# Kernel tuning notes

Hardware: AMD Instinct MI355X
Metric: run time of the kernel (lower is better)

The kernel has to match this reference:

```python
import jax, jax.numpy as jnp
import numpy as np

H = 256          # hidden_size
D = 2 * H        # GRU state size
ODE_H = 128      # ode_hidden_dim
IN_U = 32        # input_size - 1 (dt channel stripped)
OUT = 16         # output_size
L, B = 128, 1024


def setup_inputs() -> dict:
    key = jax.random.key(0)
    ks = jax.random.split(key, 16)
    s = lambda k, shape, fan: jax.random.normal(k, shape, jnp.float32) * (1.0 / np.sqrt(fan))
    ext = jax.random.uniform(ks[0], (L, B, IN_U + 1), jnp.float32)  # last channel = dt > 0
    obs = jax.random.normal(ks[1], (L, B, OUT), jnp.float32)
    return {
        "external_input_seq": ext,
        "observations_seq": obs,
        # PreProcess (Linear + tanh)
        "Wu": s(ks[2], (IN_U, H), IN_U), "bu": jnp.zeros((H,), jnp.float32),
        "Wx": s(ks[3], (OUT, H), OUT), "bx": jnp.zeros((H,), jnp.float32),
        # GRUCell(2H -> 2H), torch layout: [3*D, D]
        "W_ih": s(ks[4], (3 * D, D), D), "W_hh": s(ks[5], (3 * D, D), D),
        "b_ih": jnp.zeros((3 * D,), jnp.float32), "b_hh": jnp.zeros((3 * D,), jnp.float32),
        # ODE gradient net: Linear(H,ODE_H) -> tanh -> Linear(ODE_H,H)
        "W1": s(ks[6], (H, ODE_H), H), "b1": jnp.zeros((ODE_H,), jnp.float32),
        "W2": s(ks[7], (ODE_H, H), ODE_H), "b2": jnp.zeros((H,), jnp.float32),
        # Ly: Linear(2H, OUT)
        "WLy": s(ks[8], (D, OUT), D), "bLy": jnp.zeros((OUT,), jnp.float32),
    }


def _forward(external_input_seq, observations_seq, Wu, bu, Wx, bx,
             W_ih, W_hh, b_ih, b_hh, W1, b1, W2, b2, WLy, bLy):
    ext = external_input_seq[..., :-1]            # (L,B,IN_U)
    dt = external_input_seq[..., -1]              # (L,B)
    u_emb = jnp.tanh(ext @ Wu + bu)               # (L,B,H)
    x_emb = jnp.tanh(observations_seq @ Wx + bx)  # (L,B,H)

    def gru(x, h):
        gi = x @ W_ih.T + b_ih                    # (B,3D)
        gh = h @ W_hh.T + b_hh
        r = jax.nn.sigmoid(gi[:, :D] + gh[:, :D])
        z = jax.nn.sigmoid(gi[:, D:2 * D] + gh[:, D:2 * D])
        n = jnp.tanh(gi[:, 2 * D:] + r * gh[:, 2 * D:])
        return (1.0 - z) * n + z * h

    def step(hn, inp):
        u_t, x_t, dt_t = inp
        hn_new = gru(jnp.concatenate([u_t, x_t], axis=-1), hn)
        h, c = hn_new[:, :H], hn_new[:, H:]
        # Euler ODE step over [0, dt]: h <- h + dt * f(h)
        f = jnp.tanh(h @ W1 + b1) @ W2 + b2
        h = h + dt_t[:, None] * f
        hn_out = jnp.concatenate([h, c], axis=-1)
        return hn_out, hn  # h_seq collects carry BEFORE update (h_seq[:-1] semantics)

    hn0 = jnp.zeros((external_input_seq.shape[1], D), external_input_seq.dtype)
    _, h_seq = jax.lax.scan(step, hn0, (u_emb, x_emb, dt))  # (L,B,D)
    x_seq = h_seq @ WLy + bLy                               # (L,B,OUT) == state_mu
    return x_seq


def reference(external_input_seq, observations_seq, Wu, bu, Wx, bx,
              W_ih, W_hh, b_ih, b_hh, W1, b1, W2, b2, WLy, bLy):
    return _forward(external_input_seq, observations_seq, Wu, bu, Wx, bx,
                    W_ih, W_hh, b_ih, b_hh, W1, b1, W2, b2, WLy, bLy)
```

## Files before the change

### kernel.cpp

```cpp
#include <hip/hip_runtime.h>

#define LSEQ 128
#define BATCH 1024
#define DDIM 512
#define G3 1536
#define HS ((size_t)BATCH * DDIM)
#define INV2048 4.8828125e-4f
#define WST 520

typedef _Float16 h8 __attribute__((ext_vector_type(8)));
typedef float floatx4 __attribute__((ext_vector_type(4)));

#define MFMA16(acc, A, B) acc = __builtin_amdgcn_mfma_f32_16x16x32_f16(A, B, acc, 0, 0, 0)

__device__ __forceinline__ void fsplitS(float x, _Float16* hi, _Float16* lo) {
    _Float16 h = (_Float16)x;
    *hi = h;
    *lo = (_Float16)((x - (float)h) * 2048.0f);
}

#define BAR_LEAF(i) ((i) * 32)
#define BAR_MID(i)  ((64 + (i)) * 32)
#define BAR_ROOT    (72 * 32)
#define BAR_GEN     (73 * 32)
#define BAR_WORDS   4096

__device__ __forceinline__ void grid_bar(unsigned* bar, int blk, unsigned epoch) {
    __syncthreads();
    if (threadIdx.x == 0) {
        __builtin_amdgcn_fence(__ATOMIC_RELEASE, "agent");
        const int leaf = blk >> 2;
        unsigned v = __hip_atomic_fetch_add(bar + BAR_LEAF(leaf), 1u, __ATOMIC_ACQ_REL, __HIP_MEMORY_SCOPE_AGENT);
        if (v + 1u == epoch * 4u) {
            const int mid = leaf >> 3;
            unsigned m = __hip_atomic_fetch_add(bar + BAR_MID(mid), 1u, __ATOMIC_ACQ_REL, __HIP_MEMORY_SCOPE_AGENT);
            if (m + 1u == epoch * 8u) {
                unsigned r = __hip_atomic_fetch_add(bar + BAR_ROOT, 1u, __ATOMIC_ACQ_REL, __HIP_MEMORY_SCOPE_AGENT);
                if (r + 1u == epoch * 8u) {
                    __hip_atomic_store(bar + BAR_GEN, epoch, __ATOMIC_RELEASE, __HIP_MEMORY_SCOPE_AGENT);
                }
            }
        }
        while (__hip_atomic_load(bar + BAR_GEN, __ATOMIC_RELAXED, __HIP_MEMORY_SCOPE_AGENT) < epoch)
            __builtin_amdgcn_s_sleep(2);
        __builtin_amdgcn_fence(__ATOMIC_ACQUIRE, "agent");
    }
    __syncthreads();
}

__global__ void prep_kernel(const float* __restrict__ Wih,
                            const float* __restrict__ W1, const float* __restrict__ W2,
                            const float* __restrict__ WLy,
                            _Float16* __restrict__ Wih_lo,
                            _Float16* __restrict__ W1T_hi, _Float16* __restrict__ W1T_lo,
                            _Float16* __restrict__ W2T_hi, _Float16* __restrict__ W2T_lo,
                            _Float16* __restrict__ WLyT_hi, _Float16* __restrict__ WLyT_lo,
                            float* __restrict__ hn_f32, _Float16* __restrict__ hn_hi,
                            _Float16* __restrict__ hn_lo, unsigned* __restrict__ bar)
{
    int tid = blockIdx.x * 256 + threadIdx.x;
    for (int i = tid; i < G3 * DDIM; i += 65536) { _Float16 h; fsplitS(Wih[i], &h, &Wih_lo[i]); }
    for (int i = tid; i < 128 * 256; i += 65536) { int n = i >> 8, k = i & 255; fsplitS(W1[k * 128 + n], &W1T_hi[i], &W1T_lo[i]); }
    for (int i = tid; i < 256 * 128; i += 65536) { int n = i >> 7, k = i & 127; fsplitS(W2[k * 256 + n], &W2T_hi[i], &W2T_lo[i]); }
    for (int i = tid; i < 16 * 512;  i += 65536) { int n = i >> 9, k = i & 511; fsplitS(WLy[k * 16 + n], &WLyT_hi[i], &WLyT_lo[i]); }
    for (int i = tid; i < BATCH * DDIM; i += 65536) { hn_f32[i] = 0.f; hn_hi[i] = (_Float16)0.f; hn_lo[i] = (_Float16)0.f; }
    for (int i = tid; i < BAR_WORDS; i += 65536) bar[i] = 0u;
}

__device__ __forceinline__ void embed_rows(const float* __restrict__ ext, const float* __restrict__ obs,
                                           const float* __restrict__ Wu, const float* __restrict__ bu,
                                           const float* __restrict__ Wx, const float* __restrict__ bx,
                                           int t, int r0, int tid, float* stg,
                                           _Float16* __restrict__ oh, _Float16* __restrict__ ol)
{
    for (int i = tid; i < 256; i += 512) stg[i] = ext[((size_t)t * BATCH + r0 + (i >> 5)) * 33 + (i & 31)];
    for (int i = tid; i < 128; i += 512) stg[256 + i] = obs[((size_t)t * BATCH + r0 + (i >> 4)) * 16 + (i & 15)];
    __syncthreads();
    int c = tid;
    if (c < 256) {
        float wv[32];
        #pragma unroll
        for (int k = 0; k < 32; ++k) wv[k] = Wu[k * 256 + c];
        float b = bu[c];
        for (int r = 0; r < 8; ++r) {
            float acc = b;
            #pragma unroll
            for (int k = 0; k < 32; ++k) acc += stg[r * 32 + k] * wv[k];
            size_t p = (size_t)(r0 + r) * DDIM + c;
            fsplitS(tanhf(acc), &oh[p], &ol[p]);
        }
    } else {
        int cc = c - 256;
        float wv[16];
        #pragma unroll
        for (int k = 0; k < 16; ++k) wv[k] = Wx[k * 256 + cc];
        float b = bx[cc];
        for (int r = 0; r < 8; ++r) {
            float acc = b;
            #pragma unroll
            for (int k = 0; k < 16; ++k) acc += stg[256 + r * 16 + k] * wv[k];
            size_t p = (size_t)(r0 + r) * DDIM + c;
            fsplitS(tanhf(acc), &oh[p], &ol[p]);
        }
    }
}

__global__ void embed0_kernel(const float* __restrict__ ext, const float* __restrict__ obs,
                              const float* __restrict__ Wu, const float* __restrict__ bu,
                              const float* __restrict__ Wx, const float* __restrict__ bx,
                              _Float16* __restrict__ xcb_hi, _Float16* __restrict__ xcb_lo)
{
    __shared__ float stg[384];
    embed_rows(ext, obs, Wu, bu, Wx, bx, 0, blockIdx.x * 8, threadIdx.x, stg, xcb_hi, xcb_lo);
}

struct MainArgs {
    const float* ext;
    const float* obs;
    const float* Wu; const float* bu;
    const float* Wx; const float* bx;
    const float* Wih;
    const float* Whh;
    const float* b_ih;
    const float* b_hh;
    const float* b1;
    const float* b2;
    const float* bLy;
    const _Float16* Wih_lo;
    const _Float16* W1T_hi; const _Float16* W1T_lo;
    const _Float16* W2T_hi; const _Float16* W2T_lo;
    const _Float16* WLyT_hi; const _Float16* WLyT_lo;
    _Float16* xcb_hi; _Float16* xcb_lo;
    float* hn_f32;
    _Float16* hn_hi; _Float16* hn_lo;
    float* bufB;
    float* out;
    unsigned* bar;
};

__global__ void __launch_bounds__(512, 1) main_kernel(MainArgs a)
{
    __shared__ _Float16 sWhhHi[48 * WST];
    __shared__ _Float16 sWhhLo[48 * WST];
    __shared__ _Float16 sWihHi[48 * WST];
    __shared__ _Float16 sZ1[2 * 16 * 136];

    const int blk  = blockIdx.x;
    const int gb   = blk >> 5;
    const int gn   = blk & 31;
    const int tid  = threadIdx.x;
    const int lane = tid & 63;
    const int w    = tid >> 6;
    const int l15  = lane & 15;
    const int l4   = lane >> 4;
    const int row0 = gb * 128;
    const int arow = row0 + w * 16 + l15;
    const int j0   = gn * 16;

    for (int i = tid; i < 48 * 512; i += 512) {
        int p = i >> 9, k = i & 511;
        int grow = (p >> 4) * 512 + j0 + (p & 15);
        float wv = a.Whh[(size_t)grow * DDIM + k];
        _Float16 hi = (_Float16)wv;
        sWhhHi[p * WST + k] = hi;
        sWhhLo[p * WST + k] = (_Float16)((wv - (float)hi) * 2048.0f);
        sWihHi[p * WST + k] = (_Float16)a.Wih[(size_t)grow * DDIM + k];
    }
    __syncthreads();

    const int jc = j0 + l15;
    const float bR  = a.b_ih[jc]        + a.b_hh[jc];
    const float bZ  = a.b_ih[512 + jc]  + a.b_hh[512 + jc];
    const float bNI = a.b_ih[1024 + jc];
    const float bNH = a.b_hh[1024 + jc];
    const float bly = a.bLy[l15];
    const float b1c  = a.b1[w * 16 + l15];
    const float b2c0 = a.b2[(2 * w) * 16 + l15];
    const float b2c1 = a.b2[(2 * w + 1) * 16 + l15];
    const _Float16* pWLoR = a.Wih_lo + (size_t)(jc) * DDIM;
    const _Float16* pWLoZ = a.Wih_lo + (size_t)(512 + jc) * DDIM;
    const _Float16* pWLoN = a.Wih_lo + (size_t)(1024 + jc) * DDIM;
    const _Float16* pLyH  = a.WLyT_hi + (size_t)l15 * DDIM;
    const _Float16* pLyL  = a.WLyT_lo + (size_t)l15 * DDIM;
    const _Float16* sWiR = sWihHi + l15 * WST;
    const _Float16* sWiZ = sWihHi + (16 + l15) * WST;
    const _Float16* sWiN = sWihHi + (32 + l15) * WST;
    const _Float16* sWhRh = sWhhHi + l15 * WST;
    const _Float16* sWhZh = sWhhHi + (16 + l15) * WST;
    const _Float16* sWhNh = sWhhHi + (32 + l15) * WST;
    const _Float16* sWhRl = sWhhLo + l15 * WST;
    const _Float16* sWhZl = sWhhLo + (16 + l15) * WST;
    const _Float16* sWhNl = sWhhLo + (32 + l15) * WST;

    unsigned epoch = 0;

    for (int t = 0; t < LSEQ; ++t) {
        const int cur = t & 1, nxt = cur ^ 1;

        floatx4 aR={0.f,0.f,0.f,0.f}, aZ={0.f,0.f,0.f,0.f}, aNI={0.f,0.f,0.f,0.f}, aNH={0.f,0.f,0.f,0.f};
        floatx4 cR={0.f,0.f,0.f,0.f}, cZ={0.f,0.f,0.f,0.f}, cNI={0.f,0.f,0.f,0.f}, cNH={0.f,0.f,0.f,0.f};
        floatx4 y={0.f,0.f,0.f,0.f}, yc={0.f,0.f,0.f,0.f};

        const _Float16* xh = a.xcb_hi + (size_t)cur * HS + (size_t)arow * DDIM;
        const _Float16* xl = a.xcb_lo + (size_t)cur * HS + (size_t)arow * DDIM;
        const _Float16* hh = a.hn_hi  + (size_t)cur * HS + (size_t)arow * DDIM;
        const _Float16* hl = a.hn_lo  + (size_t)cur * HS + (size_t)arow * DDIM;

        for (int kk = 0; kk < 16; ++kk) {
            const int k = kk * 32 + l4 * 8;
            h8 Axh = *(const h8*)(xh + k);
            h8 Axl = *(const h8*)(xl + k);
            h8 BRh = *(const h8*)(sWiR + k);
            h8 BZh = *(const h8*)(sWiZ + k);
            h8 BNh = *(const h8*)(sWiN + k);
            h8 BRl = *(const h8*)(pWLoR + k);
            h8 BZl = *(const h8*)(pWLoZ + k);
            h8 BNl = *(const h8*)(pWLoN + k);
            MFMA16(aR, Axh, BRh);  MFMA16(aZ, Axh, BZh);  MFMA16(aNI, Axh, BNh);
            MFMA16(cR, Axh, BRl);  MFMA16(cR, Axl, BRh);
            MFMA16(cZ, Axh, BZl);  MFMA16(cZ, Axl, BZh);
            MFMA16(cNI, Axh, BNl); MFMA16(cNI, Axl, BNh);
        }
        if (gn == 0) {
            for (int kk = 0; kk < 16; ++kk) {
                const int k = kk * 32 + l4 * 8;
                h8 Ahh = *(const h8*)(hh + k);
                h8 Ahl = *(const h8*)(hl + k);
                h8 WRh = *(const h8*)(sWhRh + k);
                h8 WZh = *(const h8*)(sWhZh + k);
                h8 WNh = *(const h8*)(sWhNh + k);
                h8 WRl = *(const h8*)(sWhRl + k);
                h8 WZl = *(const h8*)(sWhZl + k);
                h8 WNl = *(const h8*)(sWhNl + k);
                MFMA16(aR, Ahh, WRh);  MFMA16(aZ, Ahh, WZh);  MFMA16(aNH, Ahh, WNh);
                MFMA16(cR, Ahh, WRl);  MFMA16(cR, Ahl, WRh);
                MFMA16(cZ, Ahh, WZl);  MFMA16(cZ, Ahl, WZh);
                MFMA16(cNH, Ahh, WNl); MFMA16(cNH, Ahl, WNh);
                h8 Lyh = *(const h8*)(pLyH + k);
                h8 Lyl = *(const h8*)(pLyL + k);
                MFMA16(y, Ahh, Lyh); MFMA16(yc, Ahh, Lyl); MFMA16(yc, Ahl, Lyh);
            }
        } else {
            for (int kk = 0; kk < 16; ++kk) {
                const int k = kk * 32 + l4 * 8;
                h8 Ahh = *(const h8*)(hh + k);
                h8 Ahl = *(const h8*)(hl + k);
                h8 WRh = *(const h8*)(sWhRh + k);
                h8 WZh = *(const h8*)(sWhZh + k);
                h8 WNh = *(const h8*)(sWhNh + k);
                h8 WRl = *(const h8*)(sWhRl + k);
                h8 WZl = *(const h8*)(sWhZl + k);
                h8 WNl = *(const h8*)(sWhNl + k);
                MFMA16(aR, Ahh, WRh);  MFMA16(aZ, Ahh, WZh);  MFMA16(aNH, Ahh, WNh);
                MFMA16(cR, Ahh, WRl);  MFMA16(cR, Ahl, WRh);
                MFMA16(cZ, Ahh, WZl);  MFMA16(cZ, Ahl, WZh);
                MFMA16(cNH, Ahh, WNl); MFMA16(cNH, Ahl, WNh);
            }
        }

        #pragma unroll
        for (int r = 0; r < 4; ++r) {
            int grow = row0 + w * 16 + l4 * 4 + r;
            size_t off = (size_t)grow * DDIM + jc;
            float gr  = aR[r]  + cR[r]  * INV2048 + bR;
            float gz  = aZ[r]  + cZ[r]  * INV2048 + bZ;
            float gni = aNI[r] + cNI[r] * INV2048 + bNI;
            float gnh = aNH[r] + cNH[r] * INV2048 + bNH;
            float r_ = 1.f / (1.f + expf(-gr));
            float z_ = 1.f / (1.f + expf(-gz));
            float n_ = tanhf(gni + r_ * gnh);
            float v = (1.f - z_) * n_ + z_ * a.hn_f32[cur * HS + off];
            a.bufB[off] = v;
            if (gn >= 16) {
                a.hn_f32[nxt * HS + off] = v;
                fsplitS(v, &a.hn_hi[nxt * HS + off], &a.hn_lo[nxt * HS + off]);
            }
        }
        if (gn == 0) {
            #pragma unroll
            for (int r = 0; r < 4; ++r) {
                int grow = row0 + w * 16 + l4 * 4 + r;
                a.out[((size_t)t * BATCH + grow) * 16 + l15] = y[r] + yc[r] * INV2048 + bly;
            }
        }

        if (t == LSEQ - 1) break;
        grid_bar(a.bar, blk, ++epoch);

        if (blk < 64) {
            const int prow0 = blk * 16;
            _Float16* sZ1hi = sZ1;
            _Float16* sZ1lo = sZ1 + 16 * 136;
            {
                floatx4 z = {0.f,0.f,0.f,0.f}, zc = {0.f,0.f,0.f,0.f};
                for (int kk = 0; kk < 8; ++kk) {
                    int k = kk * 32 + l4 * 8;
                    const float* pb = a.bufB + (size_t)(prow0 + l15) * DDIM + k;
                    floatx4 w0 = *(const floatx4*)pb;
                    floatx4 w1 = *(const floatx4*)(pb + 4);
                    h8 ah, al;
                    #pragma unroll
                    for (int e = 0; e < 4; ++e) {
                        _Float16 h1 = (_Float16)w0[e]; ah[e] = h1; al[e] = (_Float16)((w0[e] - (float)h1) * 2048.f);
                        _Float16 h2 = (_Float16)w1[e]; ah[4 + e] = h2; al[4 + e] = (_Float16)((w1[e] - (float)h2) * 2048.f);
                    }
                    h8 bh = *(const h8*)(a.W1T_hi + (size_t)(w * 16 + l15) * 256 + k);
                    h8 bl = *(const h8*)(a.W1T_lo + (size_t)(w * 16 + l15) * 256 + k);
                    MFMA16(z, ah, bh); MFMA16(zc, ah, bl); MFMA16(zc, al, bh);
                }
                #pragma unroll
                for (int r = 0; r < 4; ++r) {
                    int row = l4 * 4 + r, col = w * 16 + l15;
                    float zv = tanhf(z[r] + zc[r] * INV2048 + b1c);
                    fsplitS(zv, &sZ1hi[row * 136 + col], &sZ1lo[row * 136 + col]);
                }
            }
            __syncthreads();
            {
                floatx4 f0 = {0.f,0.f,0.f,0.f}, f0c = {0.f,0.f,0.f,0.f};
                floatx4 f1 = {0.f,0.f,0.f,0.f}, f1c = {0.f,0.f,0.f,0.f};
                for (int kk = 0; kk < 4; ++kk) {
                    int k = kk * 32 + l4 * 8;
                    h8 ah = *(const h8*)(sZ1hi + l15 * 136 + k);
                    h8 al = *(const h8*)(sZ1lo + l15 * 136 + k);
                    h8 b0h = *(const h8*)(a.W2T_hi + (size_t)((2 * w) * 16 + l15) * 128 + k);
                    h8 b0l = *(const h8*)(a.W2T_lo + (size_t)((2 * w) * 16 + l15) * 128 + k);
                    h8 b1h = *(const h8*)(a.W2T_hi + (size_t)((2 * w + 1) * 16 + l15) * 128 + k);
                    h8 b1l = *(const h8*)(a.W2T_lo + (size_t)((2 * w + 1) * 16 + l15) * 128 + k);
                    MFMA16(f0, ah, b0h); MFMA16(f0c, ah, b0l); MFMA16(f0c, al, b0h);
                    MFMA16(f1, ah, b1h); MFMA16(f1c, ah, b1l); MFMA16(f1c, al, b1h);
                }
                float dts[4];
                #pragma unroll
                for (int r = 0; r < 4; ++r)
                    dts[r] = a.ext[((size_t)t * BATCH + prow0 + l4 * 4 + r) * 33 + 32];
                #pragma unroll
                for (int i2 = 0; i2 < 2; ++i2) {
                    int col = (2 * w + i2) * 16 + l15;
                    floatx4 fv  = i2 ? f1 : f0;
                    floatx4 fvc = i2 ? f1c : f0c;
                    float b2v = i2 ? b2c1 : b2c0;
                    #pragma unroll
                    for (int r = 0; r < 4; ++r) {
                        size_t off = (size_t)(prow0 + l4 * 4 + r) * DDIM + col;
                        float hnew = a.bufB[off] + dts[r] * (fv[r] + fvc[r] * INV2048 + b2v);
                        a.hn_f32[nxt * HS + off] = hnew;
                        fsplitS(hnew, &a.hn_hi[nxt * HS + off], &a.hn_lo[nxt * HS + off]);
                    }
                }
            }
        } else if (blk < 192) {
            embed_rows(a.ext, a.obs, a.Wu, a.bu, a.Wx, a.bx, t + 1, (blk - 64) * 8, tid,
                       (float*)sZ1, a.xcb_hi + (size_t)nxt * HS, a.xcb_lo + (size_t)nxt * HS);
        }
        grid_bar(a.bar, blk, ++epoch);
    }
}

extern "C" void kernel_launch(void* const* d_in, const int* in_sizes, int n_in,
                              void* d_out, int out_size, void* d_ws, size_t ws_size,
                              hipStream_t stream)
{
    (void)in_sizes; (void)n_in; (void)out_size; (void)ws_size;
    const float* ext = (const float*)d_in[0];
    const float* obs = (const float*)d_in[1];
    const float* Wu  = (const float*)d_in[2];
    const float* bu  = (const float*)d_in[3];
    const float* Wx  = (const float*)d_in[4];
    const float* bx  = (const float*)d_in[5];
    const float* Wih = (const float*)d_in[6];
    const float* Whh = (const float*)d_in[7];
    const float* bih = (const float*)d_in[8];
    const float* bhh = (const float*)d_in[9];
    const float* W1  = (const float*)d_in[10];
    const float* b1  = (const float*)d_in[11];
    const float* W2  = (const float*)d_in[12];
    const float* b2  = (const float*)d_in[13];
    const float* WLy = (const float*)d_in[14];
    const float* bLy = (const float*)d_in[15];
    float* out = (float*)d_out;

    char* ws = (char*)d_ws;
    size_t off = 0;
    auto alloc = [&](size_t bytes) -> char* {
        char* p = ws + off;
        off += (bytes + 255) & ~(size_t)255;
        return p;
    };
    _Float16* xcb_hi = (_Float16*)alloc(2 * HS * 2);
    _Float16* xcb_lo = (_Float16*)alloc(2 * HS * 2);
    _Float16* Wih_lo = (_Float16*)alloc((size_t)G3 * DDIM * 2);
    _Float16* W1T_hi = (_Float16*)alloc(128 * 256 * 2);
    _Float16* W1T_lo = (_Float16*)alloc(128 * 256 * 2);
    _Float16* W2T_hi = (_Float16*)alloc(256 * 128 * 2);
    _Float16* W2T_lo = (_Float16*)alloc(256 * 128 * 2);
    _Float16* WLyT_hi = (_Float16*)alloc(16 * 512 * 2);
    _Float16* WLyT_lo = (_Float16*)alloc(16 * 512 * 2);
    float*    hn_f32 = (float*)alloc(2 * HS * 4);
    _Float16* hn_hi  = (_Float16*)alloc(2 * HS * 2);
    _Float16* hn_lo  = (_Float16*)alloc(2 * HS * 2);
    float*    bufB   = (float*)alloc(HS * 4);
    unsigned* bar    = (unsigned*)alloc(BAR_WORDS * 4);

    prep_kernel<<<256, 256, 0, stream>>>(Wih, W1, W2, WLy,
                                         Wih_lo, W1T_hi, W1T_lo, W2T_hi, W2T_lo,
                                         WLyT_hi, WLyT_lo, hn_f32, hn_hi, hn_lo, bar);
    embed0_kernel<<<128, 512, 0, stream>>>(ext, obs, Wu, bu, Wx, bx, xcb_hi, xcb_lo);

    MainArgs args;
    args.ext = ext; args.obs = obs;
    args.Wu = Wu; args.bu = bu; args.Wx = Wx; args.bx = bx;
    args.Wih = Wih; args.Whh = Whh; args.b_ih = bih; args.b_hh = bhh;
    args.b1 = b1; args.b2 = b2; args.bLy = bLy;
    args.Wih_lo = Wih_lo;
    args.W1T_hi = W1T_hi; args.W1T_lo = W1T_lo;
    args.W2T_hi = W2T_hi; args.W2T_lo = W2T_lo;
    args.WLyT_hi = WLyT_hi; args.WLyT_lo = WLyT_lo;
    args.xcb_hi = xcb_hi; args.xcb_lo = xcb_lo;
    args.hn_f32 = hn_f32; args.hn_hi = hn_hi; args.hn_lo = hn_lo;
    args.bufB = bufB; args.out = out;
    args.bar = bar;
    void* kargs[] = { &args };
    hipLaunchCooperativeKernel((const void*)main_kernel, dim3(256), dim3(512), kargs, 0, stream);
}
```

Baseline: 9.703 ms.

## Replace grid-wide barriers with per-XCD group barriers over batch row groups

Each block reads its XCD id and claims a slot, so every 128-row batch group is served by the 32 blocks on one XCD. The two per-step grid-wide barriers become group-local barriers, and the ODE and embedding work is re-split so each group handles only its own rows. The aim is to cut barrier latency and cross-XCD coherence traffic. If the XCD mapping is not uniform, a mode flag falls back to the original block-index mapping, at the cost of two extra grid barriers at startup.

```diff
diff --git a/kernel.cpp b/kernel.cpp
--- a/kernel.cpp
+++ b/kernel.cpp
@@ -23,7 +23,11 @@
 #define BAR_MID(i)  ((64 + (i)) * 32)
 #define BAR_ROOT    (72 * 32)
 #define BAR_GEN     (73 * 32)
-#define BAR_WORDS   4096
+#define BAR_WORDS   8192
+#define GB_BASE(g)  (4096 + (g) * 256)
+#define XCD_CNT(x)  (7168 + (x) * 32)
+#define MODE_FLAG   7936
+#define HWREG_XCC_ID_IMM (20 | (31 << 11))
 
 __device__ __forceinline__ void grid_bar(unsigned* bar, int blk, unsigned epoch) {
     __syncthreads();
@@ -36,12 +40,29 @@
             unsigned m = __hip_atomic_fetch_add(bar + BAR_MID(mid), 1u, __ATOMIC_ACQ_REL, __HIP_MEMORY_SCOPE_AGENT);
             if (m + 1u == epoch * 8u) {
                 unsigned r = __hip_atomic_fetch_add(bar + BAR_ROOT, 1u, __ATOMIC_ACQ_REL, __HIP_MEMORY_SCOPE_AGENT);
-                if (r + 1u == epoch * 8u) {
+                if (r + 1u == epoch * 8u)
                     __hip_atomic_store(bar + BAR_GEN, epoch, __ATOMIC_RELEASE, __HIP_MEMORY_SCOPE_AGENT);
-                }
             }
         }
         while (__hip_atomic_load(bar + BAR_GEN, __ATOMIC_RELAXED, __HIP_MEMORY_SCOPE_AGENT) < epoch)
+            __builtin_amdgcn_s_sleep(2);
+        __builtin_amdgcn_fence(__ATOMIC_ACQUIRE, "agent");
+    }
+    __syncthreads();
+}
+
+__device__ __forceinline__ void group_bar(unsigned* bar, int group, int mem, unsigned epoch) {
+    __syncthreads();
+    if (threadIdx.x == 0) {
+        __builtin_amdgcn_fence(__ATOMIC_RELEASE, "agent");
+        unsigned* g = bar + GB_BASE(group);
+        unsigned v = __hip_atomic_fetch_add(g + (mem >> 3) * 32, 1u, __ATOMIC_ACQ_REL, __HIP_MEMORY_SCOPE_AGENT);
+        if (v + 1u == epoch * 8u) {
+            unsigned r = __hip_atomic_fetch_add(g + 128, 1u, __ATOMIC_ACQ_REL, __HIP_MEMORY_SCOPE_AGENT);
+            if (r + 1u == epoch * 4u)
+                __hip_atomic_store(g + 160, epoch, __ATOMIC_RELEASE, __HIP_MEMORY_SCOPE_AGENT);
+        }
+        while (__hip_atomic_load(g + 160, __ATOMIC_RELAXED, __HIP_MEMORY_SCOPE_AGENT) < epoch)
             __builtin_amdgcn_s_sleep(2);
         __builtin_amdgcn_fence(__ATOMIC_ACQUIRE, "agent");
     }
@@ -144,18 +165,41 @@
     __shared__ _Float16 sWhhLo[48 * WST];
     __shared__ _Float16 sWihHi[48 * WST];
     __shared__ _Float16 sZ1[2 * 16 * 136];
+    __shared__ int sGroup, sMem;
 
     const int blk  = blockIdx.x;
-    const int gb   = blk >> 5;
-    const int gn   = blk & 31;
     const int tid  = threadIdx.x;
     const int lane = tid & 63;
     const int w    = tid >> 6;
     const int l15  = lane & 15;
     const int l4   = lane >> 4;
-    const int row0 = gb * 128;
-    const int arow = row0 + w * 16 + l15;
-    const int j0   = gn * 16;
+    unsigned* bar  = a.bar;
+
+    if (tid == 0) {
+        unsigned xcd = __builtin_amdgcn_s_getreg(HWREG_XCC_ID_IMM) & 0xFu;
+        if (xcd > 7u) xcd = (unsigned)(blk & 7);
+        unsigned slot = __hip_atomic_fetch_add(bar + XCD_CNT(xcd), 1u, __ATOMIC_ACQ_REL, __HIP_MEMORY_SCOPE_AGENT);
+        sGroup = (int)xcd; sMem = (int)slot;
+    }
+    grid_bar(bar, blk, 1);
+    if (blk == 0 && tid == 0) {
+        unsigned ok = 1;
+        for (int x = 0; x < 8; ++x)
+            ok &= (__hip_atomic_load(bar + XCD_CNT(x), __ATOMIC_RELAXED, __HIP_MEMORY_SCOPE_AGENT) == 32u);
+        __hip_atomic_store(bar + MODE_FLAG, ok, __ATOMIC_RELEASE, __HIP_MEMORY_SCOPE_AGENT);
+    }
+    grid_bar(bar, blk, 2);
+    if (tid == 0) {
+        unsigned mode = __hip_atomic_load(bar + MODE_FLAG, __ATOMIC_RELAXED, __HIP_MEMORY_SCOPE_AGENT);
+        if (mode == 0u || sMem > 31) { sGroup = blk >> 5; sMem = blk & 31; }
+    }
+    __syncthreads();
+    const int group = sGroup;
+    const int mem   = sMem;
+    const int gn    = mem;
+    const int row0  = group * 128;
+    const int arow  = row0 + w * 16 + l15;
+    const int j0    = gn * 16;
 
     for (int i = tid; i < 48 * 512; i += 512) {
         int p = i >> 9, k = i & 511;
@@ -285,10 +329,10 @@
         }
 
         if (t == LSEQ - 1) break;
-        grid_bar(a.bar, blk, ++epoch);
-
-        if (blk < 64) {
-            const int prow0 = blk * 16;
+        group_bar(bar, group, mem, ++epoch);
+
+        if (mem < 8) {
+            const int prow0 = row0 + mem * 16;
             _Float16* sZ1hi = sZ1;
             _Float16* sZ1lo = sZ1 + 16 * 136;
             {
@@ -349,11 +393,11 @@
                     }
                 }
             }
-        } else if (blk < 192) {
-            embed_rows(a.ext, a.obs, a.Wu, a.bu, a.Wx, a.bx, t + 1, (blk - 64) * 8, tid,
+        } else if (mem < 24) {
+            embed_rows(a.ext, a.obs, a.Wu, a.bu, a.Wx, a.bx, t + 1, row0 + (mem - 8) * 8, tid,
                        (float*)sZ1, a.xcb_hi + (size_t)nxt * HS, a.xcb_lo + (size_t)nxt * HS);
         }
-        grid_bar(a.bar, blk, ++epoch);
+        group_bar(bar, group, mem, ++epoch);
     }
 }
 
```

Result: faster. 8.977 ms (-7.5%).
